# Kernel optimization log

Measured on AMD Instinct MI355X. Metric: run time of the kernel, lower is better.

The kernel has to match this reference:

```python
import jax, jax.numpy as jnp
import numpy as np

B, S, D, H, L, FF, V, T = 4, 160, 512, 8, 2, 2048, 50000, 256
Wd = D // H


def layer_norm(x, g, b, eps=1e-12):
    u = x.mean(-1, keepdims=True)
    s = ((x - u) ** 2).mean(-1, keepdims=True)
    return g * (x - u) / jnp.sqrt(s + eps) + b


def setup_inputs() -> dict:
    key = jax.random.key(0)
    ks = jax.random.split(key, 16)
    sc = 0.02
    inp = {
        'x': jax.random.randint(ks[0], (B, S), 0, V),
        'stamp': jax.random.randint(ks[1], (B, S - 1, 3), 0, 8),
        'mask': jnp.ones((B, S), dtype=jnp.int32),
        'time_matrix': jax.random.randint(ks[2], (B, S, S), 0, T + 1),
        'tok_emb': jax.random.normal(ks[3], (V, D)) * sc,
        'month_emb': jax.random.normal(ks[4], (13, D)) * sc,
        'day_emb': jax.random.normal(ks[5], (32, D)) * sc,
        'tiK_emb': jax.random.normal(ks[6], (T + 1, D)) * sc,
        'tiV_emb': jax.random.normal(ks[7], (T + 1, D)) * sc,
        'g0': jnp.ones((D,)), 'b0': jnp.zeros((D,)),
        'Wq': jax.random.normal(ks[8], (L, D, D)) * sc, 'bq': jnp.zeros((L, D)),
        'Wk': jax.random.normal(ks[9], (L, D, D)) * sc, 'bk': jnp.zeros((L, D)),
        'Wv': jax.random.normal(ks[10], (L, D, D)) * sc, 'bv': jnp.zeros((L, D)),
        'Wo': jax.random.normal(ks[11], (L, D, D)) * sc, 'bo': jnp.zeros((L, D)),
        'g1': jnp.ones((L, D)), 'b1': jnp.zeros((L, D)),
        'W1': jax.random.normal(ks[12], (L, D, FF)) * sc, 'c1': jnp.zeros((L, FF)),
        'W2': jax.random.normal(ks[13], (L, FF, D)) * sc, 'c2': jnp.zeros((L, D)),
        'g2': jnp.ones((L, D)), 'b2': jnp.zeros((L, D)),
    }
    return inp


def reference(x, stamp, mask, time_matrix, tok_emb, month_emb, day_emb,
              tiK_emb, tiV_emb, g0, b0, Wq, bq, Wk, bk, Wv, bv, Wo, bo,
              g1, b1, W1, c1, W2, c2, g2, b2):
    # Embeddings: month + day temporal embed, one zero timestep prepended
    t_e = month_emb[stamp[..., 0]] + day_emb[stamp[..., 1]]          # [B,S-1,D]
    t_e = jnp.concatenate([jnp.zeros((B, 1, D), t_e.dtype), t_e], axis=1)
    h = layer_norm(tok_emb[x] + t_e, g0, b0)                         # [B,S,D]
    tK = tiK_emb[time_matrix].reshape(B, S, S, H, Wd)                # [B,S,S,H,W]
    tV = tiV_emb[time_matrix].reshape(B, S, S, H, Wd)
    maskf = mask.astype(h.dtype)
    # faithful to original: +10000*(1-mask), added AFTER scaling
    bias = 10000.0 * (1.0 - maskf)[:, None, None, :]
    inv_sqrt = 1.0 / jnp.sqrt(jnp.asarray(Wd, h.dtype))
    for l in range(L):
        q = (h @ Wq[l] + bq[l]).reshape(B, S, H, Wd).transpose(0, 2, 1, 3)  # [B,H,S,W]
        k = (h @ Wk[l] + bk[l]).reshape(B, S, H, Wd).transpose(0, 2, 1, 3)
        v = (h @ Wv[l] + bv[l]).reshape(B, S, H, Wd).transpose(0, 2, 1, 3)
        scores = (jnp.einsum('bhiw,bhjw->bhij', q, k)
                  + jnp.einsum('bijhw,bhiw->bhij', tK, q)) * inv_sqrt + bias
        attn = jax.nn.softmax(scores, axis=-1)                        # [B,H,S,S]
        # standard value mix + diagonal of attn-weighted t_V (relative-time values)
        hh = (jnp.einsum('bhij,bhjw->bihw', attn, v)
              + jnp.einsum('bhik,bikhw->bihw', attn, tV)).reshape(B, S, D)
        h = layer_norm(h + hh @ Wo[l] + bo[l], g1[l], b1[l])
        ff = jax.nn.gelu(h @ W1[l] + c1[l], approximate=False) @ W2[l] + c2[l]
        h = layer_norm(h + ff, g2[l], b2[l])
    return h
```

## Files before the change

### kernel.cpp

```cpp
#include <hip/hip_runtime.h>
#include <hip/hip_bf16.h>
#include <math.h>

#define SS 160
#define DD 512
#define HH 8
#define MTOK 640
#define FFD 2048
#define NTT 257

typedef __attribute__((ext_vector_type(8))) short bfrag8;
typedef __attribute__((ext_vector_type(4))) float facc4;
typedef unsigned short u16;

#define SWZ(row, cb) ((cb) ^ (((row)&7) << 4))

__device__ __forceinline__ void gload16(const void* g, void* l) {
  __builtin_amdgcn_global_load_lds(
      (const __attribute__((address_space(1))) void*)g,
      (__attribute__((address_space(3))) void*)l, 16, 0, 0);
}

__device__ void wconv_body(const float* __restrict__ src,
                           __hip_bfloat16* __restrict__ dst,
                           int K, int N, int dls, int rowoff,
                           int l, int bx, int by, float (*tile)[65])
{
  src += (size_t)l * K * N;
  dst += (size_t)l * dls + (size_t)rowoff * K;
  int k0 = by * 64, n0 = bx * 64;
  int t = threadIdx.x;
  int r = t >> 2, c0 = (t & 3) * 16;
  #pragma unroll
  for (int j = 0; j < 16; j += 4) {
    float4 v4 = *(const float4*)&src[(size_t)(k0 + r) * N + n0 + c0 + j];
    tile[r][c0 + j + 0] = v4.x; tile[r][c0 + j + 1] = v4.y;
    tile[r][c0 + j + 2] = v4.z; tile[r][c0 + j + 3] = v4.w;
  }
  __syncthreads();
  union { u16 u[8]; uint4 v; } pk;
  #pragma unroll
  for (int half = 0; half < 2; ++half) {
    #pragma unroll
    for (int j = 0; j < 8; ++j) {
      __hip_bfloat16 hb = __float2bfloat16(tile[c0 + half * 8 + j][r]);
      pk.u[j] = *reinterpret_cast<u16*>(&hb);
    }
    *(uint4*)&dst[(size_t)(n0 + r) * K + k0 + c0 + half * 8] = pk.v;
  }
}

__global__ __launch_bounds__(256) void prep_all(
    const float* __restrict__ Wq, const float* __restrict__ Wk,
    const float* __restrict__ Wv, const float* __restrict__ Wo,
    const float* __restrict__ W1, const float* __restrict__ W2,
    const float* __restrict__ tiK,
    __hip_bfloat16* __restrict__ wqkv, __hip_bfloat16* __restrict__ wo_t,
    __hip_bfloat16* __restrict__ w1_t, __hip_bfloat16* __restrict__ w2_t,
    __hip_bfloat16* __restrict__ tikb,
    const int* __restrict__ x, const int* __restrict__ stamp,
    const float* __restrict__ tok, const float* __restrict__ month,
    const float* __restrict__ day, const float* __restrict__ g0,
    const float* __restrict__ b0, float* __restrict__ h,
    __hip_bfloat16* __restrict__ hb)
{
  __shared__ float tile[64][65];
  __shared__ float ssh[4], qsh[4];
  int idx = blockIdx.x;
  int tid = threadIdx.x;

  if (idx < 1536) {
    if (idx < 384) {
      int grp = idx / 128, r = idx % 128;
      int l = r / 64, t = r % 64;
      const float* src = grp == 0 ? Wq : (grp == 1 ? Wk : Wv);
      wconv_body(src, wqkv, 512, 512, 1536 * 512, 512 * grp, l, t % 8, t / 8, tile);
    } else if (idx < 512) {
      int r = idx - 384; int l = r / 64, t = r % 64;
      wconv_body(Wo, wo_t, 512, 512, 512 * 512, 0, l, t % 8, t / 8, tile);
    } else if (idx < 1024) {
      int r = idx - 512; int l = r / 256, t = r % 256;
      wconv_body(W1, w1_t, 512, 2048, 2048 * 512, 0, l, t % 32, t / 32, tile);
    } else {
      int r = idx - 1024; int l = r / 256, t = r % 256;
      wconv_body(W2, w2_t, 2048, 512, 512 * 2048, 0, l, t % 8, t / 8, tile);
    }
  } else if (idx < 1665) {
    int i = (idx - 1536) * 256 + tid;
    if (i < NTT * DD / 4) {
      float4 v = *(const float4*)(tiK + (size_t)i * 4);
      union { u16 u[4]; uint2 w; } pk;
      __hip_bfloat16 h0 = __float2bfloat16(v.x), h1 = __float2bfloat16(v.y);
      __hip_bfloat16 h2 = __float2bfloat16(v.z), h3 = __float2bfloat16(v.w);
      pk.u[0] = *(u16*)&h0; pk.u[1] = *(u16*)&h1;
      pk.u[2] = *(u16*)&h2; pk.u[3] = *(u16*)&h3;
      *(uint2*)(tikb + (size_t)i * 4) = pk.w;
    }
  } else {
    int m = idx - 1665;
    int b = m / SS, s = m % SS, t = tid;
    int tokid = x[m];
    float v0 = tok[tokid * DD + t];
    float v1 = tok[tokid * DD + t + 256];
    if (s > 0) {
      int sidx = (b * (SS - 1) + (s - 1)) * 3;
      int mo = stamp[sidx + 0], dy = stamp[sidx + 1];
      v0 += month[mo * DD + t]       + day[dy * DD + t];
      v1 += month[mo * DD + t + 256] + day[dy * DD + t + 256];
    }
    float sum = v0 + v1, sq = v0 * v0 + v1 * v1;
    #pragma unroll
    for (int off = 1; off < 64; off <<= 1) {
      sum += __shfl_xor(sum, off);
      sq  += __shfl_xor(sq , off);
    }
    if ((t & 63) == 0) { ssh[t >> 6] = sum; qsh[t >> 6] = sq; }
    __syncthreads();
    float fsum = ssh[0] + ssh[1] + ssh[2] + ssh[3];
    float fsq  = qsh[0] + qsh[1] + qsh[2] + qsh[3];
    float u = fsum * (1.0f / 512.0f);
    float var = fsq * (1.0f / 512.0f) - u * u;
    float r = rsqrtf(var + 1e-12f);
    float y0 = g0[t]       * ((v0 - u) * r) + b0[t];
    float y1 = g0[t + 256] * ((v1 - u) * r) + b0[t + 256];
    h[m * DD + t]        = y0;  h[m * DD + t + 256]  = y1;
    hb[m * DD + t]       = __float2bfloat16(y0);
    hb[m * DD + t + 256] = __float2bfloat16(y1);
  }
}

__global__ __launch_bounds__(256) void ln_kernel(
    const float* __restrict__ in, const float* __restrict__ g,
    const float* __restrict__ b, float* __restrict__ out,
    __hip_bfloat16* __restrict__ outb)
{
  int m = blockIdx.x; int t = threadIdx.x;
  float v0 = in[m*DD + t];
  float v1 = in[m*DD + t + 256];
  float sum = v0+v1, sq = v0*v0+v1*v1;
  #pragma unroll
  for (int off=1; off<64; off<<=1) {
    sum += __shfl_xor(sum, off);
    sq  += __shfl_xor(sq , off);
  }
  __shared__ float ssh[4], qsh[4];
  if ((t&63)==0) { ssh[t>>6]=sum; qsh[t>>6]=sq; }
  __syncthreads();
  float fsum = ssh[0]+ssh[1]+ssh[2]+ssh[3];
  float fsq  = qsh[0]+qsh[1]+qsh[2]+qsh[3];
  float u = fsum * (1.0f/512.0f);
  float var = fsq * (1.0f/512.0f) - u*u;
  float r = rsqrtf(var + 1e-12f);
  float y0 = g[t]    *((v0-u)*r) + b[t];
  float y1 = g[t+256]*((v1-u)*r) + b[t+256];
  out[m*DD+t]     = y0;
  out[m*DD+t+256] = y1;
  if (outb) {
    outb[m*DD+t]     = __float2bfloat16(y0);
    outb[m*DD+t+256] = __float2bfloat16(y1);
  }
}

#define EPI_RESID 1
#define EPI_GELU 2
#define EPI_QKV 3

template<int EPI, int K>
__global__ __launch_bounds__(256) void gemm_ck(
    const __hip_bfloat16* __restrict__ A,
    const __hip_bfloat16* __restrict__ Bt,
    const float* __restrict__ bias,
    const float* __restrict__ bias2,
    const float* __restrict__ bias3,
    const float* __restrict__ resid,
    float* __restrict__ Cf,
    __hip_bfloat16* __restrict__ Cb,
    int N)
{
  constexpr int KC = 128;
  constexpr int NCH = K / KC;
  __shared__ u16 As[2][64 * KC];
  __shared__ u16 Bs[2][64 * KC];
  const int tid = threadIdx.x, wv = tid >> 6, lane = tid & 63;
  const int m0 = blockIdx.y * 64, n0 = blockIdx.x * 64;
  const int wr = wv >> 1, wc = wv & 1;
  const int fr = lane & 15, fks = lane >> 4;

  const int ldsq = (wv * 4) * 1024;
  const int off0 = ldsq + lane * 16;

  #define STAGE(c, buf) do {                                                  \
    _Pragma("unroll")                                                         \
    for (int i_ = 0; i_ < 4; ++i_) {                                          \
      int ldso = ldsq + i_ * 1024;                                            \
      int off = off0 + i_ * 1024;                                             \
      int r_ = off >> 8;                                                      \
      int p_ = off & 255;                                                     \
      int ps_ = p_ ^ ((r_ & 7) << 4);                                         \
      gload16((const char*)A  + ((size_t)(m0 + r_) * K + (c) * KC) * 2 + ps_, \
              (char*)&As[buf][0] + ldso);                                     \
      gload16((const char*)Bt + ((size_t)(n0 + r_) * K + (c) * KC) * 2 + ps_, \
              (char*)&Bs[buf][0] + ldso);                                     \
    }                                                                         \
  } while (0)

  facc4 acc[2][2] = {};
  STAGE(0, 0);
  STAGE(1, 1);

  #pragma unroll
  for (int c = 0; c < NCH; ++c) {
    if (c + 1 < NCH) asm volatile("s_waitcnt vmcnt(8)\n\ts_barrier" ::: "memory");
    else             asm volatile("s_waitcnt vmcnt(0)\n\ts_barrier" ::: "memory");
    const char* ab = (const char*)&As[c & 1][0];
    const char* bb = (const char*)&Bs[c & 1][0];
    #pragma unroll
    for (int ks = 0; ks < 4; ++ks) {
      bfrag8 af[2], bfv[2];
      #pragma unroll
      for (int mf = 0; mf < 2; ++mf) {
        int rA = wr * 32 + mf * 16 + fr;
        af[mf] = *(const bfrag8*)(ab + rA * 256 + SWZ(rA, ks * 64 + fks * 16));
      }
      #pragma unroll
      for (int nf = 0; nf < 2; ++nf) {
        int rB = wc * 32 + nf * 16 + fr;
        bfv[nf] = *(const bfrag8*)(bb + rB * 256 + SWZ(rB, ks * 64 + fks * 16));
      }
      #pragma unroll
      for (int mf = 0; mf < 2; ++mf)
        #pragma unroll
        for (int nf = 0; nf < 2; ++nf)
          acc[mf][nf] = __builtin_amdgcn_mfma_f32_16x16x32_bf16(
              af[mf], bfv[nf], acc[mf][nf], 0, 0, 0);
    }
    asm volatile("s_barrier" ::: "memory");
    if (c + 2 < NCH) STAGE(c + 2, c & 1);
  }
  #undef STAGE

  #pragma unroll
  for (int mf = 0; mf < 2; ++mf) {
    #pragma unroll
    for (int nf = 0; nf < 2; ++nf) {
      int col = n0 + wc * 32 + nf * 16 + fr;
      float bb;
      if (EPI == EPI_QKV)
        bb = col < 512 ? bias[col] : (col < 1024 ? bias2[col - 512] : bias3[col - 1024]);
      else
        bb = bias[col];
      #pragma unroll
      for (int j = 0; j < 4; ++j) {
        int row = m0 + wr * 32 + mf * 16 + fks * 4 + j;
        float c = acc[mf][nf][j] + bb;
        if (EPI == EPI_RESID) {
          c += resid[(size_t)row * N + col];
          Cf[(size_t)row * N + col] = c;
        } else {
          if (EPI == EPI_GELU) c = 0.5f * c * (1.0f + erff(c * 0.70710678118654752f));
          Cb[(size_t)row * N + col] = __float2bfloat16(c);
        }
      }
    }
  }
}

__global__ __launch_bounds__(256) void skg_kernel(
    const __hip_bfloat16* __restrict__ qkv,
    const __hip_bfloat16* __restrict__ tikb,
    float* __restrict__ Sk, float* __restrict__ G)
{
  __shared__ u16 As[64 * 64];
  __shared__ u16 Bs[64 * 64];
  const int tid = threadIdx.x;
  const int wid = tid >> 6, lane = tid & 63;
  const int wr = wid >> 1, wc = wid & 1;
  const int fr = lane & 15, fks = lane >> 4;
  const int sr = tid >> 2, sc = (tid & 3) * 16;
  const int swz0 = sr * 128 + SWZ(sr, sc * 2);
  const int swz1 = sr * 128 + SWZ(sr, sc * 2 + 16);
  int idx = blockIdx.x;

  if (idx < 288) {
    const int z = idx / 9, rem = idx % 9;
    const int m0 = (rem / 3) * 64, n0 = (rem % 3) * 64;
    const int b = z >> 3, h = z & 7;
    const __hip_bfloat16* Aq = qkv + (size_t)b * SS * 1536 + h * 64;
    const __hip_bfloat16* Bt = qkv + (size_t)b * SS * 1536 + 512 + h * 64;
    float* C = Sk + (size_t)z * SS * SS;
    const int ar = min(m0 + sr, SS - 1), br = min(n0 + sr, SS - 1);
    uint4 av0 = *(const uint4*)(Aq + (size_t)ar * 1536 + sc);
    uint4 av1 = *(const uint4*)(Aq + (size_t)ar * 1536 + sc + 8);
    uint4 bv0 = *(const uint4*)(Bt + (size_t)br * 1536 + sc);
    uint4 bv1 = *(const uint4*)(Bt + (size_t)br * 1536 + sc + 8);
    *(uint4*)((char*)As + swz0) = av0;
    *(uint4*)((char*)As + swz1) = av1;
    *(uint4*)((char*)Bs + swz0) = bv0;
    *(uint4*)((char*)Bs + swz1) = bv1;
    __syncthreads();
    facc4 acc[2][2] = {};
    #pragma unroll
    for (int ks = 0; ks < 2; ++ks) {
      bfrag8 af[2], bfv[2];
      #pragma unroll
      for (int mf = 0; mf < 2; ++mf) {
        int rA = wr * 32 + mf * 16 + fr;
        af[mf] = *(const bfrag8*)((const char*)As + rA * 128 + SWZ(rA, 64 * ks + 16 * fks));
      }
      #pragma unroll
      for (int nf = 0; nf < 2; ++nf) {
        int rB = wc * 32 + nf * 16 + fr;
        bfv[nf] = *(const bfrag8*)((const char*)Bs + rB * 128 + SWZ(rB, 64 * ks + 16 * fks));
      }
      #pragma unroll
      for (int mf = 0; mf < 2; ++mf)
        #pragma unroll
        for (int nf = 0; nf < 2; ++nf)
          acc[mf][nf] = __builtin_amdgcn_mfma_f32_16x16x32_bf16(
              af[mf], bfv[nf], acc[mf][nf], 0, 0, 0);
    }
    #pragma unroll
    for (int mf = 0; mf < 2; ++mf)
      #pragma unroll
      for (int nf = 0; nf < 2; ++nf) {
        int col = n0 + wc * 32 + nf * 16 + fr;
        #pragma unroll
        for (int j = 0; j < 4; ++j) {
          int row = m0 + wr * 32 + mf * 16 + fks * 4 + j;
          if (row < SS && col < SS) C[row * SS + col] = acc[mf][nf][j];
        }
      }
  } else {
    int i2 = idx - 288;
    const int nb = i2 % 5, mb = (i2 / 5) % 10, h = i2 / 50;
    const int m0 = mb * 64, n0 = nb * 64;
    const __hip_bfloat16* Aq = qkv + h * 64;
    const __hip_bfloat16* Bt = tikb + h * 64;
    const int br = min(n0 + sr, NTT - 1);
    uint4 av0 = *(const uint4*)(Aq + (size_t)(m0 + sr) * 1536 + sc);
    uint4 av1 = *(const uint4*)(Aq + (size_t)(m0 + sr) * 1536 + sc + 8);
    uint4 bv0 = *(const uint4*)(Bt + (size_t)br * 512 + sc);
    uint4 bv1 = *(const uint4*)(Bt + (size_t)br * 512 + sc + 8);
    *(uint4*)((char*)As + swz0) = av0;
    *(uint4*)((char*)As + swz1) = av1;
    *(uint4*)((char*)Bs + swz0) = bv0;
    *(uint4*)((char*)Bs + swz1) = bv1;
    __syncthreads();
    facc4 acc[2][2] = {};
    #pragma unroll
    for (int ks = 0; ks < 2; ++ks) {
      bfrag8 af[2], bfv[2];
      #pragma unroll
      for (int mf = 0; mf < 2; ++mf) {
        int rA = wr * 32 + mf * 16 + fr;
        af[mf] = *(const bfrag8*)((const char*)As + rA * 128 + SWZ(rA, 64 * ks + 16 * fks));
      }
      #pragma unroll
      for (int nf = 0; nf < 2; ++nf) {
        int rB = wc * 32 + nf * 16 + fr;
        bfv[nf] = *(const bfrag8*)((const char*)Bs + rB * 128 + SWZ(rB, 64 * ks + 16 * fks));
      }
      #pragma unroll
      for (int mf = 0; mf < 2; ++mf)
        #pragma unroll
        for (int nf = 0; nf < 2; ++nf)
          acc[mf][nf] = __builtin_amdgcn_mfma_f32_16x16x32_bf16(
              af[mf], bfv[nf], acc[mf][nf], 0, 0, 0);
    }
    #pragma unroll
    for (int mf = 0; mf < 2; ++mf)
      #pragma unroll
      for (int nf = 0; nf < 2; ++nf) {
        int col = n0 + wc * 32 + nf * 16 + fr;
        #pragma unroll
        for (int j = 0; j < 4; ++j) {
          int row = m0 + wr * 32 + mf * 16 + fks * 4 + j;
          if (col < NTT)
            G[((size_t)h * MTOK + row) * NTT + col] = acc[mf][nf][j];
        }
      }
  }
}

__global__ __launch_bounds__(256) void attn2(
    const __hip_bfloat16* __restrict__ qkv,
    const float* __restrict__ Sk, const float* __restrict__ G,
    const int* __restrict__ tm, const int* __restrict__ mask,
    const float* __restrict__ tiV, __hip_bfloat16* __restrict__ hh)
{
  const int h = blockIdx.y, b = blockIdx.z;
  const int ib0 = blockIdx.x * 8;
  const int tid = threadIdx.x, wv = tid >> 6, lane = tid & 63;
  __shared__ float P[8][176];
  __shared__ int tmsh[8][176];

  float rinvs[2];
  #pragma unroll
  for (int rr = 0; rr < 2; ++rr) {
    const int r = wv * 2 + rr, i = ib0 + r, m = b * SS + i;
    const float* Grow = G + ((size_t)h * MTOK + m) * NTT;
    const float* Srow = Sk + ((size_t)(b * 8 + h) * SS + i) * SS;
    const int* tmrow = tm + (size_t)m * SS;
    float sv[3];
    float mx = -1e30f;
    #pragma unroll
    for (int g = 0; g < 3; ++g) {
      int j = lane + g * 64;
      if (j < SS) {
        int t = tmrow[j];
        tmsh[r][j] = t;
        float s = (Srow[j] + Grow[t]) * 0.125f
                + 10000.0f * (1.0f - (float)mask[b * SS + j]);
        sv[g] = s; mx = fmaxf(mx, s);
      } else sv[g] = -1e30f;
    }
    #pragma unroll
    for (int off = 1; off < 64; off <<= 1) mx = fmaxf(mx, __shfl_xor(mx, off));
    float sum = 0.f;
    #pragma unroll
    for (int g = 0; g < 3; ++g) {
      int j = lane + g * 64;
      if (j < SS) { float p = expf(sv[g] - mx); P[r][j] = p; sum += p; }
    }
    #pragma unroll
    for (int off = 1; off < 64; off <<= 1) sum += __shfl_xor(sum, off);
    rinvs[rr] = 1.0f / sum;
  }

  const int r0 = wv * 2, r1 = r0 + 1;
  const int i0 = ib0 + r0, i1 = ib0 + r1;
  const __hip_bfloat16* vbase = qkv + (size_t)b * SS * 1536 + 1024 + h * 64 + lane;
  const float* tvbase = tiV + h * 64 + lane;
  float acc0 = 0.f, acc1 = 0.f;
  #pragma unroll 4
  for (int j = 0; j < SS; ++j) {
    float vv = __bfloat162float(vbase[(size_t)j * 1536]);
    float a0 = P[r0][j], a1 = P[r1][j];
    int t0 = tmsh[r0][j], t1 = tmsh[r1][j];
    acc0 += a0 * (vv + tvbase[(size_t)t0 * 512]);
    acc1 += a1 * (vv + tvbase[(size_t)t1 * 512]);
  }
  hh[((size_t)(b * SS) + i0) * DD + h * 64 + lane] = __float2bfloat16(acc0 * rinvs[0]);
  hh[((size_t)(b * SS) + i1) * DD + h * 64 + lane] = __float2bfloat16(acc1 * rinvs[1]);
}

extern "C" void kernel_launch(void* const* d_in, const int* in_sizes, int n_in,
                              void* d_out, int out_size, void* d_ws, size_t ws_size,
                              hipStream_t stream) {
  const int*   x     = (const int*)d_in[0];
  const int*   stamp = (const int*)d_in[1];
  const int*   mask  = (const int*)d_in[2];
  const int*   tm    = (const int*)d_in[3];
  const float* tok   = (const float*)d_in[4];
  const float* month = (const float*)d_in[5];
  const float* day   = (const float*)d_in[6];
  const float* tiK   = (const float*)d_in[7];
  const float* tiV   = (const float*)d_in[8];
  const float* g0    = (const float*)d_in[9];
  const float* b0    = (const float*)d_in[10];
  const float* Wq    = (const float*)d_in[11];
  const float* bq    = (const float*)d_in[12];
  const float* Wk    = (const float*)d_in[13];
  const float* bk    = (const float*)d_in[14];
  const float* Wv    = (const float*)d_in[15];
  const float* bv    = (const float*)d_in[16];
  const float* Wo    = (const float*)d_in[17];
  const float* bo    = (const float*)d_in[18];
  const float* g1    = (const float*)d_in[19];
  const float* b1    = (const float*)d_in[20];
  const float* W1    = (const float*)d_in[21];
  const float* c1    = (const float*)d_in[22];
  const float* W2    = (const float*)d_in[23];
  const float* c2    = (const float*)d_in[24];
  const float* g2    = (const float*)d_in[25];
  const float* b2    = (const float*)d_in[26];

  float* out = (float*)d_out;
  const size_t NT = (size_t)MTOK * DD;

  char* p = (char*)d_ws;
  float* h    = (float*)p;  p += NT * 4;
  float* tb   = (float*)p;  p += NT * 4;
  float* Skb  = (float*)p;  p += (size_t)32 * SS * SS * 4;
  float* Gb   = (float*)p;  p += (size_t)HH * MTOK * NTT * 4;
  __hip_bfloat16* h_bf   = (__hip_bfloat16*)p;  p += NT * 2;
  __hip_bfloat16* hh_bf  = (__hip_bfloat16*)p;  p += NT * 2;
  __hip_bfloat16* fb_bf  = (__hip_bfloat16*)p;  p += (size_t)MTOK * FFD * 2;
  __hip_bfloat16* qkv_bf = (__hip_bfloat16*)p;  p += (size_t)MTOK * 1536 * 2;
  __hip_bfloat16* tikb   = (__hip_bfloat16*)p;  p += (size_t)NTT * DD * 2;
  __hip_bfloat16* wqkv   = (__hip_bfloat16*)p;  p += (size_t)2 * 1536 * 512 * 2;
  __hip_bfloat16* wo_t   = (__hip_bfloat16*)p;  p += (size_t)2 * 512 * 512 * 2;
  __hip_bfloat16* w1_t   = (__hip_bfloat16*)p;  p += (size_t)2 * 2048 * 512 * 2;
  __hip_bfloat16* w2_t   = (__hip_bfloat16*)p;  p += (size_t)2 * 512 * 2048 * 2;

  prep_all<<<2305, 256, 0, stream>>>(Wq, Wk, Wv, Wo, W1, W2, tiK,
                                     wqkv, wo_t, w1_t, w2_t, tikb,
                                     x, stamp, tok, month, day, g0, b0, h, h_bf);

  for (int l = 0; l < 2; ++l) {
    gemm_ck<EPI_QKV, 512><<<dim3(24, 10), 256, 0, stream>>>(
        h_bf, wqkv + (size_t)l * 1536 * 512, bq + l*DD, bk + l*DD, bv + l*DD,
        nullptr, nullptr, qkv_bf, 1536);

    skg_kernel<<<688, 256, 0, stream>>>(qkv_bf, tikb, Skb, Gb);

    attn2<<<dim3(20, 8, 4), 256, 0, stream>>>(qkv_bf, Skb, Gb, tm, mask, tiV, hh_bf);

    gemm_ck<EPI_RESID, 512><<<dim3(8, 10), 256, 0, stream>>>(
        hh_bf, wo_t + (size_t)l * 512 * 512, bo + l*DD, nullptr, nullptr,
        h, tb, nullptr, 512);
    ln_kernel<<<MTOK, 256, 0, stream>>>(tb, g1 + l*DD, b1 + l*DD, h, h_bf);

    gemm_ck<EPI_GELU, 512><<<dim3(32, 10), 256, 0, stream>>>(
        h_bf, w1_t + (size_t)l * 2048 * 512, c1 + l*FFD, nullptr, nullptr,
        nullptr, nullptr, fb_bf, 2048);

    gemm_ck<EPI_RESID, 2048><<<dim3(8, 10), 256, 0, stream>>>(
        fb_bf, w2_t + (size_t)l * 512 * 2048, c2 + l*DD, nullptr, nullptr,
        h, tb, nullptr, 512);
    ln_kernel<<<MTOK, 256, 0, stream>>>(tb, g2 + l*DD, b2 + l*DD,
                                        (l == 1) ? out : h,
                                        (l == 1) ? nullptr : h_bf);
  }
}
```

Measured before the change: 147.9 us.

## Rewrite attention value mix as MFMA GEMM over probabilities and time-bucket weights

The per-row attention output (P·V plus the gathered relative-time values) is rebuilt as one bf16 MFMA GEMM. The softmax kernel scatters each row's probabilities into 257 time-bucket sums with LDS atomics and writes them next to the raw probabilities, forming a K=448 operand. V is transposed inside the skg kernel and tiV is transposed into bf16 in the prep kernel. This replaces a scalar loop that gathered fp32 tiV rows per element, at the cost of an extra launch, LDS atomics and bf16 rounding of the probabilities.

```diff
diff --git a/kernel.cpp b/kernel.cpp
--- a/kernel.cpp
+++ b/kernel.cpp
@@ -8,6 +8,7 @@
 #define MTOK 640
 #define FFD 2048
 #define NTT 257
+#define KPW 448
 
 typedef __attribute__((ext_vector_type(8))) short bfrag8;
 typedef __attribute__((ext_vector_type(4))) float facc4;
@@ -19,6 +20,11 @@
   __builtin_amdgcn_global_load_lds(
       (const __attribute__((address_space(1))) void*)g,
       (__attribute__((address_space(3))) void*)l, 16, 0, 0);
+}
+
+__device__ __forceinline__ u16 f2b(float f) {
+  __hip_bfloat16 hb = __float2bfloat16(f);
+  return *reinterpret_cast<u16*>(&hb);
 }
 
 __device__ void wconv_body(const float* __restrict__ src,
@@ -42,10 +48,8 @@
   #pragma unroll
   for (int half = 0; half < 2; ++half) {
     #pragma unroll
-    for (int j = 0; j < 8; ++j) {
-      __hip_bfloat16 hb = __float2bfloat16(tile[c0 + half * 8 + j][r]);
-      pk.u[j] = *reinterpret_cast<u16*>(&hb);
-    }
+    for (int j = 0; j < 8; ++j)
+      pk.u[j] = f2b(tile[c0 + half * 8 + j][r]);
     *(uint4*)&dst[(size_t)(n0 + r) * K + k0 + c0 + half * 8] = pk.v;
   }
 }
@@ -54,10 +58,10 @@
     const float* __restrict__ Wq, const float* __restrict__ Wk,
     const float* __restrict__ Wv, const float* __restrict__ Wo,
     const float* __restrict__ W1, const float* __restrict__ W2,
-    const float* __restrict__ tiK,
+    const float* __restrict__ tiK, const float* __restrict__ tiV,
     __hip_bfloat16* __restrict__ wqkv, __hip_bfloat16* __restrict__ wo_t,
     __hip_bfloat16* __restrict__ w1_t, __hip_bfloat16* __restrict__ w2_t,
-    __hip_bfloat16* __restrict__ tikb,
+    __hip_bfloat16* __restrict__ tikb, __hip_bfloat16* __restrict__ tivT,
     const int* __restrict__ x, const int* __restrict__ stamp,
     const float* __restrict__ tok, const float* __restrict__ month,
     const float* __restrict__ day, const float* __restrict__ g0,
@@ -90,13 +94,11 @@
     if (i < NTT * DD / 4) {
       float4 v = *(const float4*)(tiK + (size_t)i * 4);
       union { u16 u[4]; uint2 w; } pk;
-      __hip_bfloat16 h0 = __float2bfloat16(v.x), h1 = __float2bfloat16(v.y);
-      __hip_bfloat16 h2 = __float2bfloat16(v.z), h3 = __float2bfloat16(v.w);
-      pk.u[0] = *(u16*)&h0; pk.u[1] = *(u16*)&h1;
-      pk.u[2] = *(u16*)&h2; pk.u[3] = *(u16*)&h3;
+      pk.u[0] = f2b(v.x); pk.u[1] = f2b(v.y);
+      pk.u[2] = f2b(v.z); pk.u[3] = f2b(v.w);
       *(uint2*)(tikb + (size_t)i * 4) = pk.w;
     }
-  } else {
+  } else if (idx < 2305) {
     int m = idx - 1665;
     int b = m / SS, s = m % SS, t = tid;
     int tokid = x[m];
@@ -126,6 +128,13 @@
     h[m * DD + t]        = y0;  h[m * DD + t + 256]  = y1;
     hb[m * DD + t]       = __float2bfloat16(y0);
     hb[m * DD + t + 256] = __float2bfloat16(y1);
+  } else {
+    int hd = idx - 2305;
+    for (int i2 = tid; i2 < 64 * 272; i2 += 256) {
+      int n = i2 / 272, c = i2 % 272;
+      float val = (c < NTT) ? tiV[(size_t)c * DD + hd * 64 + n] : 0.f;
+      tivT[((size_t)hd * 64 + n) * 272 + c] = __float2bfloat16(val);
+    }
   }
 }
 
@@ -268,10 +277,12 @@
 __global__ __launch_bounds__(256) void skg_kernel(
     const __hip_bfloat16* __restrict__ qkv,
     const __hip_bfloat16* __restrict__ tikb,
-    float* __restrict__ Sk, float* __restrict__ G)
+    float* __restrict__ Sk, float* __restrict__ G,
+    __hip_bfloat16* __restrict__ vT)
 {
   __shared__ u16 As[64 * 64];
   __shared__ u16 Bs[64 * 64];
+  __shared__ u16 tt[64][72];
   const int tid = threadIdx.x;
   const int wid = tid >> 6, lane = tid & 63;
   const int wr = wid >> 1, wc = wid & 1;
@@ -330,7 +341,7 @@
           if (row < SS && col < SS) C[row * SS + col] = acc[mf][nf][j];
         }
       }
-  } else {
+  } else if (idx < 688) {
     int i2 = idx - 288;
     const int nb = i2 % 5, mb = (i2 / 5) % 10, h = i2 / 50;
     const int m0 = mb * 64, n0 = nb * 64;
@@ -379,36 +390,64 @@
             G[((size_t)h * MTOK + row) * NTT + col] = acc[mf][nf][j];
         }
       }
-  }
-}
-
-__global__ __launch_bounds__(256) void attn2(
-    const __hip_bfloat16* __restrict__ qkv,
+  } else {
+    const int z = idx - 688, b = z >> 3, h = z & 7;
+    const __hip_bfloat16* vsl = qkv + (size_t)b * SS * 1536 + 1024 + h * 64;
+    const int jr = tid >> 2, nc = (tid & 3) * 16;
+    #pragma unroll
+    for (int jt = 0; jt < 3; ++jt) {
+      int j = jt * 64 + jr;
+      uint4 v0 = {0,0,0,0}, v1 = {0,0,0,0};
+      if (j < SS) {
+        v0 = *(const uint4*)(vsl + (size_t)j * 1536 + nc);
+        v1 = *(const uint4*)(vsl + (size_t)j * 1536 + nc + 8);
+      }
+      __syncthreads();
+      const u16* p0 = (const u16*)&v0;
+      const u16* p1 = (const u16*)&v1;
+      #pragma unroll
+      for (int e = 0; e < 8; ++e) {
+        tt[nc + e][jr]     = p0[e];
+        tt[nc + 8 + e][jr] = p1[e];
+      }
+      __syncthreads();
+      int n = tid >> 2, seg = (tid & 3) * 16;
+      int jbase = jt * 64 + seg;
+      if (jbase < SS) {
+        *(uint4*)(vT + ((size_t)z * 64 + n) * 160 + jbase)     = *(uint4*)&tt[n][seg];
+        *(uint4*)(vT + ((size_t)z * 64 + n) * 160 + jbase + 8) = *(uint4*)&tt[n][seg + 8];
+      }
+    }
+  }
+}
+
+__global__ __launch_bounds__(256) void attn3(
     const float* __restrict__ Sk, const float* __restrict__ G,
     const int* __restrict__ tm, const int* __restrict__ mask,
-    const float* __restrict__ tiV, __hip_bfloat16* __restrict__ hh)
+    __hip_bfloat16* __restrict__ pwA, float* __restrict__ rinvb)
 {
   const int h = blockIdx.y, b = blockIdx.z;
   const int ib0 = blockIdx.x * 8;
   const int tid = threadIdx.x, wv = tid >> 6, lane = tid & 63;
-  __shared__ float P[8][176];
-  __shared__ int tmsh[8][176];
-
-  float rinvs[2];
+  const int z = b * 8 + h;
+  __shared__ float wlds[8][272];
+
   #pragma unroll
   for (int rr = 0; rr < 2; ++rr) {
     const int r = wv * 2 + rr, i = ib0 + r, m = b * SS + i;
+    __hip_bfloat16* pArow = pwA + ((size_t)z * SS + i) * KPW;
     const float* Grow = G + ((size_t)h * MTOK + m) * NTT;
-    const float* Srow = Sk + ((size_t)(b * 8 + h) * SS + i) * SS;
+    const float* Srow = Sk + ((size_t)z * SS + i) * SS;
     const int* tmrow = tm + (size_t)m * SS;
-    float sv[3];
+    for (int c = lane; c < 272; c += 64) wlds[r][c] = 0.f;
+    int tv[3]; float sv[3];
     float mx = -1e30f;
     #pragma unroll
     for (int g = 0; g < 3; ++g) {
       int j = lane + g * 64;
       if (j < SS) {
         int t = tmrow[j];
-        tmsh[r][j] = t;
+        tv[g] = t;
         float s = (Srow[j] + Grow[t]) * 0.125f
                 + 10000.0f * (1.0f - (float)mask[b * SS + j]);
         sv[g] = s; mx = fmaxf(mx, s);
@@ -416,32 +455,108 @@
     }
     #pragma unroll
     for (int off = 1; off < 64; off <<= 1) mx = fmaxf(mx, __shfl_xor(mx, off));
-    float sum = 0.f;
+    float sum = 0.f; float pv[3];
     #pragma unroll
     for (int g = 0; g < 3; ++g) {
       int j = lane + g * 64;
-      if (j < SS) { float p = expf(sv[g] - mx); P[r][j] = p; sum += p; }
+      if (j < SS) { pv[g] = expf(sv[g] - mx); sum += pv[g]; }
     }
     #pragma unroll
     for (int off = 1; off < 64; off <<= 1) sum += __shfl_xor(sum, off);
-    rinvs[rr] = 1.0f / sum;
-  }
-
-  const int r0 = wv * 2, r1 = r0 + 1;
-  const int i0 = ib0 + r0, i1 = ib0 + r1;
-  const __hip_bfloat16* vbase = qkv + (size_t)b * SS * 1536 + 1024 + h * 64 + lane;
-  const float* tvbase = tiV + h * 64 + lane;
-  float acc0 = 0.f, acc1 = 0.f;
-  #pragma unroll 4
-  for (int j = 0; j < SS; ++j) {
-    float vv = __bfloat162float(vbase[(size_t)j * 1536]);
-    float a0 = P[r0][j], a1 = P[r1][j];
-    int t0 = tmsh[r0][j], t1 = tmsh[r1][j];
-    acc0 += a0 * (vv + tvbase[(size_t)t0 * 512]);
-    acc1 += a1 * (vv + tvbase[(size_t)t1 * 512]);
-  }
-  hh[((size_t)(b * SS) + i0) * DD + h * 64 + lane] = __float2bfloat16(acc0 * rinvs[0]);
-  hh[((size_t)(b * SS) + i1) * DD + h * 64 + lane] = __float2bfloat16(acc1 * rinvs[1]);
+    if (lane == 0) rinvb[(size_t)z * SS + i] = 1.0f / sum;
+    #pragma unroll
+    for (int g = 0; g < 3; ++g) {
+      int j = lane + g * 64;
+      if (j < SS) {
+        pArow[j] = __float2bfloat16(pv[g]);
+        atomicAdd(&wlds[r][tv[g]], pv[g]);
+      } else if (j < 176) {
+        pArow[j] = __float2bfloat16(0.f);
+      }
+    }
+    for (int c = lane; c < 272; c += 64)
+      pArow[176 + c] = __float2bfloat16(wlds[r][c]);
+  }
+}
+
+__global__ __launch_bounds__(256) void pv_gemm(
+    const __hip_bfloat16* __restrict__ pwA,
+    const __hip_bfloat16* __restrict__ vT,
+    const __hip_bfloat16* __restrict__ tivT,
+    const float* __restrict__ rinvb,
+    __hip_bfloat16* __restrict__ hh)
+{
+  const int z = blockIdx.y, b = z >> 3, h = z & 7;
+  const int m0 = blockIdx.x * 64;
+  __shared__ u16 As[64 * 64];
+  __shared__ u16 Bs[64 * 64];
+  const int tid = threadIdx.x;
+  const int wid = tid >> 6, lane = tid & 63;
+  const int wr = wid >> 1, wc = wid & 1;
+  const int fr = lane & 15, fks = lane >> 4;
+  const int sr = tid >> 2, sc = (tid & 3) * 16;
+  const int swz0 = sr * 128 + SWZ(sr, sc * 2);
+  const int swz1 = sr * 128 + SWZ(sr, sc * 2 + 16);
+  const int ar = min(m0 + sr, SS - 1);
+  const __hip_bfloat16* Arow = pwA + ((size_t)z * SS + ar) * KPW;
+  const __hip_bfloat16* vRow = vT + ((size_t)z * 64 + sr) * 160;
+  const __hip_bfloat16* tRow = tivT + ((size_t)h * 64 + sr) * 272;
+
+  facc4 acc[2][2] = {};
+  #pragma unroll
+  for (int c = 0; c < 7; ++c) {
+    int k0 = c * 64 + sc;
+    uint4 a0 = *(const uint4*)(Arow + k0);
+    uint4 a1 = *(const uint4*)(Arow + k0 + 8);
+    uint4 b0 = {0,0,0,0}, b1 = {0,0,0,0};
+    int kb = k0;
+    if (kb < 160)      b0 = *(const uint4*)(vRow + kb);
+    else if (kb >= 176) b0 = *(const uint4*)(tRow + kb - 176);
+    kb = k0 + 8;
+    if (kb < 160)      b1 = *(const uint4*)(vRow + kb);
+    else if (kb >= 176) b1 = *(const uint4*)(tRow + kb - 176);
+    __syncthreads();
+    *(uint4*)((char*)As + swz0) = a0;
+    *(uint4*)((char*)As + swz1) = a1;
+    *(uint4*)((char*)Bs + swz0) = b0;
+    *(uint4*)((char*)Bs + swz1) = b1;
+    __syncthreads();
+    #pragma unroll
+    for (int ks = 0; ks < 2; ++ks) {
+      bfrag8 af[2], bfv[2];
+      #pragma unroll
+      for (int mf = 0; mf < 2; ++mf) {
+        int rA = wr * 32 + mf * 16 + fr;
+        af[mf] = *(const bfrag8*)((const char*)As + rA * 128 + SWZ(rA, 64 * ks + 16 * fks));
+      }
+      #pragma unroll
+      for (int nf = 0; nf < 2; ++nf) {
+        int rB = wc * 32 + nf * 16 + fr;
+        bfv[nf] = *(const bfrag8*)((const char*)Bs + rB * 128 + SWZ(rB, 64 * ks + 16 * fks));
+      }
+      #pragma unroll
+      for (int mf = 0; mf < 2; ++mf)
+        #pragma unroll
+        for (int nf = 0; nf < 2; ++nf)
+          acc[mf][nf] = __builtin_amdgcn_mfma_f32_16x16x32_bf16(
+              af[mf], bfv[nf], acc[mf][nf], 0, 0, 0);
+    }
+  }
+  #pragma unroll
+  for (int mf = 0; mf < 2; ++mf)
+    #pragma unroll
+    for (int nf = 0; nf < 2; ++nf) {
+      int col = wc * 32 + nf * 16 + fr;
+      #pragma unroll
+      for (int j = 0; j < 4; ++j) {
+        int row = m0 + wr * 32 + mf * 16 + fks * 4 + j;
+        if (row < SS) {
+          float scale = rinvb[(size_t)z * SS + row];
+          hh[((size_t)(b * SS + row)) * DD + h * 64 + col] =
+              __float2bfloat16(acc[mf][nf][j] * scale);
+        }
+      }
+    }
 }
 
 extern "C" void kernel_launch(void* const* d_in, const int* in_sizes, int n_in,
@@ -483,18 +598,22 @@
   float* tb   = (float*)p;  p += NT * 4;
   float* Skb  = (float*)p;  p += (size_t)32 * SS * SS * 4;
   float* Gb   = (float*)p;  p += (size_t)HH * MTOK * NTT * 4;
+  float* rinvb= (float*)p;  p += (size_t)32 * SS * 4;
   __hip_bfloat16* h_bf   = (__hip_bfloat16*)p;  p += NT * 2;
   __hip_bfloat16* hh_bf  = (__hip_bfloat16*)p;  p += NT * 2;
   __hip_bfloat16* fb_bf  = (__hip_bfloat16*)p;  p += (size_t)MTOK * FFD * 2;
   __hip_bfloat16* qkv_bf = (__hip_bfloat16*)p;  p += (size_t)MTOK * 1536 * 2;
   __hip_bfloat16* tikb   = (__hip_bfloat16*)p;  p += (size_t)NTT * DD * 2;
+  __hip_bfloat16* tivT   = (__hip_bfloat16*)p;  p += (size_t)HH * 64 * 272 * 2;
+  __hip_bfloat16* vTb    = (__hip_bfloat16*)p;  p += (size_t)32 * 64 * 160 * 2;
+  __hip_bfloat16* pwA    = (__hip_bfloat16*)p;  p += (size_t)32 * SS * KPW * 2;
   __hip_bfloat16* wqkv   = (__hip_bfloat16*)p;  p += (size_t)2 * 1536 * 512 * 2;
   __hip_bfloat16* wo_t   = (__hip_bfloat16*)p;  p += (size_t)2 * 512 * 512 * 2;
   __hip_bfloat16* w1_t   = (__hip_bfloat16*)p;  p += (size_t)2 * 2048 * 512 * 2;
   __hip_bfloat16* w2_t   = (__hip_bfloat16*)p;  p += (size_t)2 * 512 * 2048 * 2;
 
-  prep_all<<<2305, 256, 0, stream>>>(Wq, Wk, Wv, Wo, W1, W2, tiK,
-                                     wqkv, wo_t, w1_t, w2_t, tikb,
+  prep_all<<<2313, 256, 0, stream>>>(Wq, Wk, Wv, Wo, W1, W2, tiK, tiV,
+                                     wqkv, wo_t, w1_t, w2_t, tikb, tivT,
                                      x, stamp, tok, month, day, g0, b0, h, h_bf);
 
   for (int l = 0; l < 2; ++l) {
@@ -502,9 +621,11 @@
         h_bf, wqkv + (size_t)l * 1536 * 512, bq + l*DD, bk + l*DD, bv + l*DD,
         nullptr, nullptr, qkv_bf, 1536);
 
-    skg_kernel<<<688, 256, 0, stream>>>(qkv_bf, tikb, Skb, Gb);
-
-    attn2<<<dim3(20, 8, 4), 256, 0, stream>>>(qkv_bf, Skb, Gb, tm, mask, tiV, hh_bf);
+    skg_kernel<<<720, 256, 0, stream>>>(qkv_bf, tikb, Skb, Gb, vTb);
+
+    attn3<<<dim3(20, 8, 4), 256, 0, stream>>>(Skb, Gb, tm, mask, pwA, rinvb);
+
+    pv_gemm<<<dim3(3, 32), 256, 0, stream>>>(pwA, vTb, tivT, rinvb, hh_bf);
 
     gemm_ck<EPI_RESID, 512><<<dim3(8, 10), 256, 0, stream>>>(
         hh_bf, wo_t + (size_t)l * 512 * 512, bo + l*DD, nullptr, nullptr,
```

Result: slower. 155.9 us (+5.4%).

## Fuse Wo and W2 GEMMs with residual add and LayerNorm into one kernel

Applied to the files above, without the earlier changes.

Replaces the residual GEMM plus separate LayerNorm kernels with a gemm_ln kernel. Each block owns 16 full rows and all 512 output columns across 8 waves, so the row statistics can be reduced inside the block. This removes four kernel launches and the round trip of the fp32 temporary buffer. In exchange, only 40 blocks run, the operands are loaded straight from global memory into registers without LDS staging, and the K=2048 GEMM has a long serial loop per block. That could underuse the GPU's CUs.

```diff
diff --git a/kernel.cpp b/kernel.cpp
--- a/kernel.cpp
+++ b/kernel.cpp
@@ -19,6 +19,11 @@
   __builtin_amdgcn_global_load_lds(
       (const __attribute__((address_space(1))) void*)g,
       (__attribute__((address_space(3))) void*)l, 16, 0, 0);
+}
+
+__device__ __forceinline__ u16 f2b(float f) {
+  __hip_bfloat16 hb = __float2bfloat16(f);
+  return *reinterpret_cast<u16*>(&hb);
 }
 
 __device__ void wconv_body(const float* __restrict__ src,
@@ -42,10 +47,8 @@
   #pragma unroll
   for (int half = 0; half < 2; ++half) {
     #pragma unroll
-    for (int j = 0; j < 8; ++j) {
-      __hip_bfloat16 hb = __float2bfloat16(tile[c0 + half * 8 + j][r]);
-      pk.u[j] = *reinterpret_cast<u16*>(&hb);
-    }
+    for (int j = 0; j < 8; ++j)
+      pk.u[j] = f2b(tile[c0 + half * 8 + j][r]);
     *(uint4*)&dst[(size_t)(n0 + r) * K + k0 + c0 + half * 8] = pk.v;
   }
 }
@@ -90,10 +93,8 @@
     if (i < NTT * DD / 4) {
       float4 v = *(const float4*)(tiK + (size_t)i * 4);
       union { u16 u[4]; uint2 w; } pk;
-      __hip_bfloat16 h0 = __float2bfloat16(v.x), h1 = __float2bfloat16(v.y);
-      __hip_bfloat16 h2 = __float2bfloat16(v.z), h3 = __float2bfloat16(v.w);
-      pk.u[0] = *(u16*)&h0; pk.u[1] = *(u16*)&h1;
-      pk.u[2] = *(u16*)&h2; pk.u[3] = *(u16*)&h3;
+      pk.u[0] = f2b(v.x); pk.u[1] = f2b(v.y);
+      pk.u[2] = f2b(v.z); pk.u[3] = f2b(v.w);
       *(uint2*)(tikb + (size_t)i * 4) = pk.w;
     }
   } else {
@@ -129,39 +130,6 @@
   }
 }
 
-__global__ __launch_bounds__(256) void ln_kernel(
-    const float* __restrict__ in, const float* __restrict__ g,
-    const float* __restrict__ b, float* __restrict__ out,
-    __hip_bfloat16* __restrict__ outb)
-{
-  int m = blockIdx.x; int t = threadIdx.x;
-  float v0 = in[m*DD + t];
-  float v1 = in[m*DD + t + 256];
-  float sum = v0+v1, sq = v0*v0+v1*v1;
-  #pragma unroll
-  for (int off=1; off<64; off<<=1) {
-    sum += __shfl_xor(sum, off);
-    sq  += __shfl_xor(sq , off);
-  }
-  __shared__ float ssh[4], qsh[4];
-  if ((t&63)==0) { ssh[t>>6]=sum; qsh[t>>6]=sq; }
-  __syncthreads();
-  float fsum = ssh[0]+ssh[1]+ssh[2]+ssh[3];
-  float fsq  = qsh[0]+qsh[1]+qsh[2]+qsh[3];
-  float u = fsum * (1.0f/512.0f);
-  float var = fsq * (1.0f/512.0f) - u*u;
-  float r = rsqrtf(var + 1e-12f);
-  float y0 = g[t]    *((v0-u)*r) + b[t];
-  float y1 = g[t+256]*((v1-u)*r) + b[t+256];
-  out[m*DD+t]     = y0;
-  out[m*DD+t+256] = y1;
-  if (outb) {
-    outb[m*DD+t]     = __float2bfloat16(y0);
-    outb[m*DD+t+256] = __float2bfloat16(y1);
-  }
-}
-
-#define EPI_RESID 1
 #define EPI_GELU 2
 #define EPI_QKV 3
 
@@ -172,8 +140,6 @@
     const float* __restrict__ bias,
     const float* __restrict__ bias2,
     const float* __restrict__ bias3,
-    const float* __restrict__ resid,
-    float* __restrict__ Cf,
     __hip_bfloat16* __restrict__ Cb,
     int N)
 {
@@ -253,14 +219,115 @@
       for (int j = 0; j < 4; ++j) {
         int row = m0 + wr * 32 + mf * 16 + fks * 4 + j;
         float c = acc[mf][nf][j] + bb;
-        if (EPI == EPI_RESID) {
-          c += resid[(size_t)row * N + col];
-          Cf[(size_t)row * N + col] = c;
-        } else {
-          if (EPI == EPI_GELU) c = 0.5f * c * (1.0f + erff(c * 0.70710678118654752f));
-          Cb[(size_t)row * N + col] = __float2bfloat16(c);
-        }
-      }
+        if (EPI == EPI_GELU) c = 0.5f * c * (1.0f + erff(c * 0.70710678118654752f));
+        Cb[(size_t)row * N + col] = __float2bfloat16(c);
+      }
+    }
+  }
+}
+
+template<int K>
+__global__ __launch_bounds__(512) void gemm_ln(
+    const __hip_bfloat16* __restrict__ A,
+    const __hip_bfloat16* __restrict__ Bt,
+    const float* __restrict__ bias,
+    const float* __restrict__ resid,
+    const float* __restrict__ g, const float* __restrict__ b,
+    float* __restrict__ outf,
+    __hip_bfloat16* __restrict__ outb)
+{
+  constexpr int NCH = K / 64;
+  const int tid = threadIdx.x, wv = tid >> 6, lane = tid & 63;
+  const int fr = lane & 15, fks = lane >> 4;
+  const int m0 = blockIdx.x * 16;
+  const int n0 = wv * 64;
+
+  const char* Abase = (const char*)(A + (size_t)(m0 + fr) * K);
+  const char* Bb[4];
+  #pragma unroll
+  for (int nf = 0; nf < 4; ++nf)
+    Bb[nf] = (const char*)(Bt + (size_t)(n0 + nf * 16 + fr) * K);
+
+  bfrag8 afb[2][2];
+  bfrag8 bfb[2][4][2];
+  facc4 acc[4] = {};
+
+  #define LOADC(buf, ck_) do {                                                \
+    _Pragma("unroll")                                                         \
+    for (int ks = 0; ks < 2; ++ks) {                                          \
+      afb[buf][ks] = *(const bfrag8*)(Abase + (ck_) * 128 + ks * 64 + fks * 16); \
+      _Pragma("unroll")                                                       \
+      for (int nf = 0; nf < 4; ++nf)                                          \
+        bfb[buf][nf][ks] = *(const bfrag8*)(Bb[nf] + (ck_) * 128 + ks * 64 + fks * 16); \
+    }                                                                         \
+  } while (0)
+
+  LOADC(0, 0);
+  #pragma unroll
+  for (int ck = 0; ck < NCH; ++ck) {
+    if (ck + 1 < NCH) LOADC((ck + 1) & 1, ck + 1);
+    const int cb = ck & 1;
+    #pragma unroll
+    for (int ks = 0; ks < 2; ++ks)
+      #pragma unroll
+      for (int nf = 0; nf < 4; ++nf)
+        acc[nf] = __builtin_amdgcn_mfma_f32_16x16x32_bf16(
+            afb[cb][ks], bfb[cb][nf][ks], acc[nf], 0, 0, 0);
+  }
+  #undef LOADC
+
+  float val[4][4];
+  float s[4] = {0.f, 0.f, 0.f, 0.f}, q[4] = {0.f, 0.f, 0.f, 0.f};
+  #pragma unroll
+  for (int nf = 0; nf < 4; ++nf) {
+    int col = n0 + nf * 16 + fr;
+    float bc = bias[col];
+    #pragma unroll
+    for (int j = 0; j < 4; ++j) {
+      int row = m0 + fks * 4 + j;
+      float v = acc[nf][j] + bc + resid[(size_t)row * 512 + col];
+      val[nf][j] = v;
+      s[j] += v; q[j] += v * v;
+    }
+  }
+  #pragma unroll
+  for (int off = 1; off < 16; off <<= 1) {
+    #pragma unroll
+    for (int j = 0; j < 4; ++j) {
+      s[j] += __shfl_xor(s[j], off);
+      q[j] += __shfl_xor(q[j], off);
+    }
+  }
+  __shared__ float sP[8][16], qP[8][16];
+  __shared__ float stot[16], qtot[16];
+  if (fr == 0) {
+    #pragma unroll
+    for (int j = 0; j < 4; ++j) {
+      sP[wv][fks * 4 + j] = s[j];
+      qP[wv][fks * 4 + j] = q[j];
+    }
+  }
+  __syncthreads();
+  if (tid < 16) {
+    float ss = 0.f, qq = 0.f;
+    #pragma unroll
+    for (int w = 0; w < 8; ++w) { ss += sP[w][tid]; qq += qP[w][tid]; }
+    stot[tid] = ss; qtot[tid] = qq;
+  }
+  __syncthreads();
+  #pragma unroll
+  for (int j = 0; j < 4; ++j) {
+    int rloc = fks * 4 + j;
+    int row = m0 + rloc;
+    float u = stot[rloc] * (1.0f / 512.0f);
+    float var = qtot[rloc] * (1.0f / 512.0f) - u * u;
+    float rr = rsqrtf(var + 1e-12f);
+    #pragma unroll
+    for (int nf = 0; nf < 4; ++nf) {
+      int col = n0 + nf * 16 + fr;
+      float y = g[col] * ((val[nf][j] - u) * rr) + b[col];
+      outf[(size_t)row * 512 + col] = y;
+      if (outb) outb[(size_t)row * 512 + col] = __float2bfloat16(y);
     }
   }
 }
@@ -480,7 +547,6 @@
 
   char* p = (char*)d_ws;
   float* h    = (float*)p;  p += NT * 4;
-  float* tb   = (float*)p;  p += NT * 4;
   float* Skb  = (float*)p;  p += (size_t)32 * SS * SS * 4;
   float* Gb   = (float*)p;  p += (size_t)HH * MTOK * NTT * 4;
   __hip_bfloat16* h_bf   = (__hip_bfloat16*)p;  p += NT * 2;
@@ -500,26 +566,22 @@
   for (int l = 0; l < 2; ++l) {
     gemm_ck<EPI_QKV, 512><<<dim3(24, 10), 256, 0, stream>>>(
         h_bf, wqkv + (size_t)l * 1536 * 512, bq + l*DD, bk + l*DD, bv + l*DD,
-        nullptr, nullptr, qkv_bf, 1536);
+        qkv_bf, 1536);
 
     skg_kernel<<<688, 256, 0, stream>>>(qkv_bf, tikb, Skb, Gb);
 
     attn2<<<dim3(20, 8, 4), 256, 0, stream>>>(qkv_bf, Skb, Gb, tm, mask, tiV, hh_bf);
 
-    gemm_ck<EPI_RESID, 512><<<dim3(8, 10), 256, 0, stream>>>(
-        hh_bf, wo_t + (size_t)l * 512 * 512, bo + l*DD, nullptr, nullptr,
-        h, tb, nullptr, 512);
-    ln_kernel<<<MTOK, 256, 0, stream>>>(tb, g1 + l*DD, b1 + l*DD, h, h_bf);
+    gemm_ln<512><<<40, 512, 0, stream>>>(
+        hh_bf, wo_t + (size_t)l * 512 * 512, bo + l*DD, h,
+        g1 + l*DD, b1 + l*DD, h, h_bf);
 
     gemm_ck<EPI_GELU, 512><<<dim3(32, 10), 256, 0, stream>>>(
         h_bf, w1_t + (size_t)l * 2048 * 512, c1 + l*FFD, nullptr, nullptr,
-        nullptr, nullptr, fb_bf, 2048);
-
-    gemm_ck<EPI_RESID, 2048><<<dim3(8, 10), 256, 0, stream>>>(
-        fb_bf, w2_t + (size_t)l * 512 * 2048, c2 + l*DD, nullptr, nullptr,
-        h, tb, nullptr, 512);
-    ln_kernel<<<MTOK, 256, 0, stream>>>(tb, g2 + l*DD, b2 + l*DD,
-                                        (l == 1) ? out : h,
-                                        (l == 1) ? nullptr : h_bf);
-  }
-}
+        fb_bf, 2048);
+
+    gemm_ln<2048><<<40, 512, 0, stream>>>(
+        fb_bf, w2_t + (size_t)l * 512 * 2048, c2 + l*DD, h,
+        g2 + l*DD, b2 + l*DD, (l == 1) ? out : h, (l == 1) ? nullptr : h_bf);
+  }
+}
```

New measurement: 283.7 us. 1.92x slower.
